# Performance work log

Measured on AMD Instinct MI355X. Metric: run time of the kernel, lower is better.

The kernel has to match this reference:

```python
import jax, jax.numpy as jnp
import numpy as np

B_, L_, H_, P_ = 8, 4096, 512, 256
DT_MIN, DT_MAX = 1e-3, 1e-1


def setup_inputs() -> dict:
    key = jax.random.key(0)
    ks = jax.random.split(key, 6)
    input_sequence = jax.random.normal(ks[0], (B_, L_, H_), jnp.float32)
    # Stable diagonal SSM eigenvalues (HiPPO-like): negative real, spread imaginary
    Lambda_re = -0.5 * jnp.ones((P_,), jnp.float32)
    Lambda_im = jnp.pi * jnp.arange(P_, dtype=jnp.float32)
    # B, C stored as real arrays with trailing real/imag channel, as in the module
    B = jax.random.normal(ks[1], (P_, H_, 2), jnp.float32) / np.sqrt(2.0 * H_)
    C = jax.random.normal(ks[2], (H_, P_, 2), jnp.float32) / np.sqrt(float(P_))
    D = jax.random.normal(ks[3], (H_,), jnp.float32)
    log_step = jax.random.uniform(ks[4], (P_,), jnp.float32,
                                  float(np.log(DT_MIN)), float(np.log(DT_MAX)))
    return dict(input_sequence=input_sequence, Lambda_re=Lambda_re,
                Lambda_im=Lambda_im, B=B, C=C, D=D, log_step=log_step)


def _scan_ssm(Lambda_bar, Bu):
    """Diagonal linear recurrence x_k = Lambda_bar * x_{k-1} + Bu_k via parallel scan.
    Lambda_bar: (P,) complex64; Bu: (L, P) complex64 -> xs: (L, P) complex64."""
    A = jnp.broadcast_to(Lambda_bar, Bu.shape)

    def binop(e_i, e_j):
        a_i, b_i = e_i
        a_j, b_j = e_j
        return a_j * a_i, a_j * b_i + b_j

    _, xs = jax.lax.associative_scan(binop, (A, Bu))
    return xs


def reference(input_sequence, Lambda_re, Lambda_im, B, C, D, log_step):
    # complex parameters (conj_sym=True, clip_eigs=False, zoh discretization)
    Lambda = (Lambda_re + 1j * Lambda_im).astype(jnp.complex64)        # (P,)
    B_tilde = (B[..., 0] + 1j * B[..., 1]).astype(jnp.complex64)       # (P, H)
    C_tilde = (C[..., 0] + 1j * C[..., 1]).astype(jnp.complex64)       # (H, P)
    step = jnp.exp(log_step)                                           # (P,)
    # ZOH: Lambda_bar = exp(Lambda*dt); B_bar = Lambda^{-1}(Lambda_bar - I) B
    Lambda_bar = jnp.exp(Lambda * step)                                # (P,)
    B_bar = ((1.0 / Lambda) * (Lambda_bar - 1.0))[:, None] * B_tilde   # (P, H)
    # project inputs into state space: (B, L, P)
    Bu = jnp.einsum('blh,ph->blp', input_sequence.astype(jnp.complex64), B_bar)
    xs = jax.vmap(lambda bu: _scan_ssm(Lambda_bar, bu))(Bu)            # (B, L, P)
    state = xs[:, -1, :]                                               # (B, P)
    # conj_sym=True -> output uses 2 * Re(C x)
    ys = 2.0 * jnp.einsum('blp,hp->blh', xs, C_tilde).real             # (B, L, H)
    out = ys + D * input_sequence                                      # D-skip
    return out, state
```

## Files before the change

### kernel.cpp

```cpp
#include <hip/hip_runtime.h>
#include <hip/hip_bf16.h>

#define Hh 512
#define Pp 256
#define Ll 4096
#define Bb 8
#define BL (Bb*Ll)
#define Sc 64
#define NC 64

typedef __attribute__((ext_vector_type(8))) __bf16 bf16x8;
typedef __attribute__((ext_vector_type(4))) float  floatx4;

#define LAM_OFF     0
#define LAMS64D_OFF 512
#define B1G_OFF     1024
#define B3G_OFF     (B1G_OFF + 65536)
#define UB16_OFF    (B3G_OFF + 65536)
#define BUB_OFF     (UB16_OFF + 4194304)
#define XSB_OFF     (BUB_OFF + 4194304)
#define AGG_OFF     (XSB_OFF + 4194304)

#define OUT_ELEMS 16777216

#define GLL16(g, l) __builtin_amdgcn_global_load_lds( \
    (const __attribute__((address_space(1))) void*)(g), \
    (__attribute__((address_space(3))) void*)(l), 16, 0, 0)

#define BAR_LGKM()  asm volatile("s_waitcnt lgkmcnt(0)\n\ts_barrier" ::: "memory")
#define BAR_VMN(n)  asm volatile("s_waitcnt vmcnt(" #n ")\n\ts_barrier" ::: "memory")

__device__ __forceinline__ float2 cmul(float2 a, float2 b) {
    return make_float2(a.x*b.x - a.y*b.y, a.x*b.y + a.y*b.x);
}
__device__ __forceinline__ void cfma(float2& acc, float2 a, float2 b) {
    acc.x = fmaf(a.x, b.x, acc.x); acc.x = fmaf(-a.y, b.y, acc.x);
    acc.y = fmaf(a.x, b.y, acc.y); acc.y = fmaf( a.y, b.x, acc.y);
}

__global__ void prep(const float* __restrict__ u,
                     const float* __restrict__ Bmat, const float* __restrict__ Cmat,
                     const float* __restrict__ Lre, const float* __restrict__ Lim,
                     const float* __restrict__ logstep, float2* __restrict__ ws) {
    int bid = blockIdx.x;
    if (bid < 8192) {
        long i = ((long)bid * 256 + threadIdx.x) * 8;
        float4 v0 = *(const float4*)(u + i);
        float4 v1 = *(const float4*)(u + i + 4);
        __align__(16) __hip_bfloat162 t[4];
        t[0] = __float22bfloat162_rn(make_float2(v0.x, v0.y));
        t[1] = __float22bfloat162_rn(make_float2(v0.z, v0.w));
        t[2] = __float22bfloat162_rn(make_float2(v1.x, v1.y));
        t[3] = __float22bfloat162_rn(make_float2(v1.z, v1.w));
        *(bf16x8*)((__hip_bfloat16*)(ws + UB16_OFF) + i) = *(const bf16x8*)t;
    } else if (bid < 8704) {
        int idx = (bid - 8192) * 256 + threadIdx.x;
        int p = idx >> 9, h = idx & 511;
        double lr = (double)Lre[p], li = (double)Lim[p];
        double st = exp((double)logstep[p]);
        double a  = lr * st, th = li * st;
        double er = exp(a);
        double lamr = er * cos(th), lami = er * sin(th);
        double nr = lamr - 1.0, ni = lami;
        double den = lr*lr + li*li;
        float gx = (float)((nr*lr + ni*li)/den), gy = (float)((ni*lr - nr*li)/den);
        float2 b = ((const float2*)Bmat)[idx];
        float re = gx*b.x - gy*b.y;
        float im = gx*b.y + gy*b.x;
        __hip_bfloat16* B1 = (__hip_bfloat16*)(ws + B1G_OFF);
        B1[(2*p)*512 + h]   = __float2bfloat16(re);
        B1[(2*p+1)*512 + h] = __float2bfloat16(im);
    } else if (bid < 9216) {
        int idx = (bid - 8704) * 256 + threadIdx.x;
        int h = idx >> 8, p = idx & 255;
        float2 c = ((const float2*)Cmat)[idx];
        __hip_bfloat162* B3 = (__hip_bfloat162*)(ws + B3G_OFF);
        B3[h*256 + p] = __float22bfloat162_rn(make_float2(2.f*c.x, -2.f*c.y));
    } else {
        int p = threadIdx.x;
        double lr = (double)Lre[p], li = (double)Lim[p];
        double st = exp((double)logstep[p]);
        double a  = lr * st, th = li * st;
        double er = exp(a);
        ws[LAM_OFF + p] = make_float2((float)(er*cos(th)), (float)(er*sin(th)));
        double er64 = exp(64.0 * a), th64 = 64.0 * th;
        ((double2*)(ws + LAMS64D_OFF))[p] = make_double2(er64*cos(th64), er64*sin(th64));
    }
}

#define STAGE(buf, kt) do { \
    _Pragma("unroll") \
    for (int h_ = 0; h_ < 2; ++h_) { \
        _Pragma("unroll") \
        for (int r_ = 0; r_ < 2; ++r_) { \
            GLL16(aSrc + (h_*128 + r_*64)*1024 + (kt)*128, \
                  ldsSt + (buf)*65536 + h_*16384 + r_*8192); \
            GLL16(bSrc + (h_*128 + r_*64)*1024 + (kt)*128, \
                  ldsSt + (buf)*65536 + 32768 + h_*16384 + r_*8192); \
        } \
    } \
} while (0)

template<int EPI>
__global__ __launch_bounds__(512, 2)
void gemm8(const __hip_bfloat16* __restrict__ A,
           const __hip_bfloat16* __restrict__ B,
           void* __restrict__ Cout,
           const __hip_bfloat16* __restrict__ ub,
           const float* __restrict__ Dv) {
    __shared__ __align__(16) char lds[131072];
    const int tid = threadIdx.x;
    const int w = tid >> 6, l = tid & 63;

    const int idx = blockIdx.x;
    const int swz = (idx & 7) * 32 + (idx >> 3);
    const int mt = swz >> 1, nt = swz & 1;
    const long M0 = (long)mt * 256;
    const int  N0 = nt * 256;

    const int rA  = l >> 3;
    const int csw = ((l & 7) ^ rA) * 16;
    const char* aSrc = (const char*)A + (M0 + w*8 + rA) * 1024 + csw;
    const char* bSrc = (const char*)B + (long)(N0 + w*8 + rA) * 1024 + csw;
    char* ldsSt = lds + w*1024 + l*16;

    const int quad = l >> 4, ml = l & 15, m7 = ml & 7;
    const int wm = w & 1, wn = w >> 1;
    const int o0 = ((quad    ) ^ m7) * 16;
    const int o1 = ((quad + 4) ^ m7) * 16;
    const char* aRd = lds + wm*16384 + ml*128;
    const char* bRd = lds + 32768 + (wn >> 1)*16384 + ((wn & 1)*64 + ml)*128;

    floatx4 acc[8][4];
    #pragma unroll
    for (int i = 0; i < 8; ++i)
        #pragma unroll
        for (int j = 0; j < 4; ++j) acc[i][j] = (floatx4)0.f;

    STAGE(0, 0);
    STAGE(1, 1);
    BAR_VMN(8);

    #pragma unroll
    for (int t = 0; t < 8; ++t) {
        const int tb = (t & 1) * 65536;

        {
            bf16x8 af[8], bfr[4];
            #pragma unroll
            for (int fm = 0; fm < 8; ++fm)
                af[fm] = *(const bf16x8*)(aRd + tb + fm*2048 + o0);
            #pragma unroll
            for (int fn = 0; fn < 4; ++fn)
                bfr[fn] = *(const bf16x8*)(bRd + tb + fn*2048 + o0);
            __builtin_amdgcn_s_setprio(1);
            #pragma unroll
            for (int fm = 0; fm < 8; ++fm)
                #pragma unroll
                for (int fn = 0; fn < 4; ++fn)
                    acc[fm][fn] = __builtin_amdgcn_mfma_f32_16x16x32_bf16(
                        af[fm], bfr[fn], acc[fm][fn], 0, 0, 0);
            __builtin_amdgcn_s_setprio(0);
        }

        {
            bf16x8 af[8], bfr[4];
            #pragma unroll
            for (int fm = 0; fm < 8; ++fm)
                af[fm] = *(const bf16x8*)(aRd + tb + fm*2048 + o1);
            #pragma unroll
            for (int fn = 0; fn < 4; ++fn)
                bfr[fn] = *(const bf16x8*)(bRd + tb + fn*2048 + o1);
            BAR_LGKM();
            if (t + 2 < 8) STAGE(t & 1, t + 2);
            __builtin_amdgcn_sched_barrier(0);
            __builtin_amdgcn_s_setprio(1);
            #pragma unroll
            for (int fm = 0; fm < 8; ++fm)
                #pragma unroll
                for (int fn = 0; fn < 4; ++fn)
                    acc[fm][fn] = __builtin_amdgcn_mfma_f32_16x16x32_bf16(
                        af[fm], bfr[fn], acc[fm][fn], 0, 0, 0);
            __builtin_amdgcn_s_setprio(0);
        }

        if (t < 6)       BAR_VMN(8);
        else if (t == 6) BAR_VMN(0);
    }

    #pragma unroll
    for (int fm = 0; fm < 8; ++fm)
        #pragma unroll
        for (int fn = 0; fn < 4; ++fn) {
            const int col = N0 + wn*64 + fn*16 + ml;
            const float d = (EPI == 1) ? Dv[col] : 0.f;
            #pragma unroll
            for (int reg = 0; reg < 4; ++reg) {
                const long row = M0 + wm*128 + fm*16 + quad*4 + reg;
                const long o = row * 512 + col;
                if (EPI == 0) {
                    ((__hip_bfloat16*)Cout)[o] = __float2bfloat16(acc[fm][fn][reg]);
                } else {
                    ((float*)Cout)[o] = acc[fm][fn][reg] + d * __bfloat162float(ub[o]);
                }
            }
        }
}

__global__ void k2a(float2* __restrict__ ws) {
    int p = threadIdx.x;
    int bc = blockIdx.x;
    int b = bc >> 6, c = bc & 63;
    float2 lam = ws[LAM_OFF + p];
    float2 lp[8];
    lp[0] = make_float2(1.f, 0.f);
    #pragma unroll
    for (int k = 1; k < 8; ++k) lp[k] = cmul(lp[k-1], lam);
    float2 lam8 = cmul(lp[7], lam);
    const __hip_bfloat162* __restrict__ bub = (const __hip_bfloat162*)(ws + BUB_OFF);
    long base = (long)(b*Ll + c*Sc) * Pp + p;
    float2 agg = make_float2(0.f, 0.f);
    for (int j0 = 0; j0 < Sc; j0 += 8) {
        float2 v[8];
        #pragma unroll
        for (int i = 0; i < 8; ++i)
            v[i] = __bfloat1622float2(bub[base + (long)(j0 + i) * Pp]);
        float2 s0 = make_float2(0.f, 0.f), s1 = make_float2(0.f, 0.f);
        #pragma unroll
        for (int i = 0; i < 8; i += 2) {
            cfma(s0, lp[7 - i], v[i]);
            cfma(s1, lp[6 - i], v[i + 1]);
        }
        float2 G = make_float2(s0.x + s1.x, s0.y + s1.y);
        float2 na = cmul(lam8, agg);
        agg = make_float2(na.x + G.x, na.y + G.y);
    }
    ws[AGG_OFF + bc * Pp + p] = agg;
}

__global__ void k2c(float2* __restrict__ ws, float* __restrict__ dout) {
    int p = threadIdx.x;
    int bc = blockIdx.x;
    int b = bc >> 6, c = bc & 63;
    float2 lam = ws[LAM_OFF + p];
    double2 l64 = ((const double2*)(ws + LAMS64D_OFF))[p];
    double cr = 0.0, ci = 0.0;
    for (int cp = 0; cp < c; ++cp) {
        float2 a = ws[AGG_OFF + (b*NC + cp) * Pp + p];
        double nr = fma(l64.x, cr, (double)a.x); nr = fma(-l64.y, ci, nr);
        double ni = fma(l64.x, ci, (double)a.y); ni = fma( l64.y, cr, ni);
        cr = nr; ci = ni;
    }
    float2 x = make_float2((float)cr, (float)ci);
    const __hip_bfloat162* __restrict__ bub = (const __hip_bfloat162*)(ws + BUB_OFF);
    __hip_bfloat162* __restrict__ xsb = (__hip_bfloat162*)(ws + XSB_OFF);
    long base = (long)(b*Ll + c*Sc) * Pp + p;
    for (int j0 = 0; j0 < Sc; j0 += 8) {
        float2 v[8];
        #pragma unroll
        for (int i = 0; i < 8; ++i)
            v[i] = __bfloat1622float2(bub[base + (long)(j0 + i) * Pp]);
        #pragma unroll
        for (int i = 0; i < 8; ++i) {
            float nr = fmaf(lam.x, x.x, v[i].x); nr = fmaf(-lam.y, x.y, nr);
            float ni = fmaf(lam.x, x.y, v[i].y); ni = fmaf( lam.y, x.x, ni);
            x.x = nr; x.y = ni;
            xsb[base + (long)(j0 + i) * Pp] = __float22bfloat162_rn(make_float2(x.x, x.y));
        }
    }
    if (c == NC - 1) {
        dout[OUT_ELEMS + b * Pp + p] = x.x;
        dout[OUT_ELEMS + Bb * Pp + b * Pp + p] = x.y;
    }
}

extern "C" void kernel_launch(void* const* d_in, const int* in_sizes, int n_in,
                              void* d_out, int out_size, void* d_ws, size_t ws_size,
                              hipStream_t stream) {
    const float* u       = (const float*)d_in[0];
    const float* Lre     = (const float*)d_in[1];
    const float* Lim     = (const float*)d_in[2];
    const float* Bmat    = (const float*)d_in[3];
    const float* Cmat    = (const float*)d_in[4];
    const float* Dv      = (const float*)d_in[5];
    const float* logstep = (const float*)d_in[6];
    float*  out = (float*)d_out;
    float2* ws  = (float2*)d_ws;

    prep<<<9217, 256, 0, stream>>>(u, Bmat, Cmat, Lre, Lim, logstep, ws);

    gemm8<0><<<256, 512, 0, stream>>>(
        (const __hip_bfloat16*)(ws + UB16_OFF),
        (const __hip_bfloat16*)(ws + B1G_OFF),
        (void*)(ws + BUB_OFF), nullptr, nullptr);

    k2a<<<Bb*NC, 256, 0, stream>>>(ws);
    k2c<<<Bb*NC, 256, 0, stream>>>(ws, out);

    gemm8<1><<<256, 512, 0, stream>>>(
        (const __hip_bfloat16*)(ws + XSB_OFF),
        (const __hip_bfloat16*)(ws + B3G_OFF),
        (void*)out,
        (const __hip_bfloat16*)(ws + UB16_OFF), Dv);
}
```

Measured before the change: 203.7 us.

## Fuse chunk-aggregate scan computation into first GEMM epilogue, drop k2a kernel

The per-chunk state aggregates are now computed inside the Bu GEMM epilogue, directly from the accumulator registers. Each lane weights its rows by powers of lambda and reduces across lanes with shuffles, then writes one aggregate per 64-step chunk. This removes the separate k2a launch and its re-read of the bf16 Bu buffer from global memory. In exchange the GEMM epilogue does more complex arithmetic and register work, which may lower occupancy or lengthen the tail. Summation order also changes, with lambda powers rebuilt from repeated multiplies.

```diff
diff --git a/kernel.cpp b/kernel.cpp
--- a/kernel.cpp
+++ b/kernel.cpp
@@ -107,7 +107,9 @@
            const __hip_bfloat16* __restrict__ B,
            void* __restrict__ Cout,
            const __hip_bfloat16* __restrict__ ub,
-           const float* __restrict__ Dv) {
+           const float* __restrict__ Dv,
+           const float2* __restrict__ lamTab,
+           float2* __restrict__ aggOut) {
     __shared__ __align__(16) char lds[131072];
     const int tid = threadIdx.x;
     const int w = tid >> 6, l = tid & 63;
@@ -188,54 +190,69 @@
         else if (t == 6) BAR_VMN(0);
     }
 
-    #pragma unroll
-    for (int fm = 0; fm < 8; ++fm)
+    if constexpr (EPI == 0) {
+        const int b   = (int)(M0 >> 12);
+        const int gc0 = (int)((M0 >> 6) & 63);
         #pragma unroll
         for (int fn = 0; fn < 4; ++fn) {
             const int col = N0 + wn*64 + fn*16 + ml;
-            const float d = (EPI == 1) ? Dv[col] : 0.f;
-            #pragma unroll
-            for (int reg = 0; reg < 4; ++reg) {
-                const long row = M0 + wm*128 + fm*16 + quad*4 + reg;
-                const long o = row * 512 + col;
-                if (EPI == 0) {
-                    ((__hip_bfloat16*)Cout)[o] = __float2bfloat16(acc[fm][fn][reg]);
-                } else {
+            const int p = col >> 1;
+            const float2 lam = lamTab[p];
+            const float2 one = make_float2(1.f, 0.f);
+            const float2 l2  = cmul(lam, lam);
+            const float2 l3  = cmul(l2, lam);
+            const float2 l4  = cmul(l2, l2);
+            const float2 l8  = cmul(l4, l4);
+            const float2 l12 = cmul(l8, l4);
+            const float2 l16 = cmul(l8, l8);
+            const float2 l32 = cmul(l16, l16);
+            const float2 l48 = cmul(l32, l16);
+            const float2 P4q = (quad==3) ? one : (quad==2) ? l4 : (quad==1) ? l8 : l12;
+            #pragma unroll
+            for (int c = 0; c < 2; ++c) {
+                float2 sc = make_float2(0.f, 0.f);
+                #pragma unroll
+                for (int a = 0; a < 4; ++a) {
+                    const int fm = c*4 + a;
+                    float vr[4];
+                    #pragma unroll
+                    for (int reg = 0; reg < 4; ++reg) {
+                        const long row = M0 + wm*128 + fm*16 + quad*4 + reg;
+                        __hip_bfloat16 hv = __float2bfloat16(acc[fm][fn][reg]);
+                        ((__hip_bfloat16*)Cout)[row * 512 + col] = hv;
+                        vr[reg] = __bfloat162float(hv);
+                    }
+                    float2 s;
+                    s.x = fmaf(l3.x, vr[0], fmaf(l2.x, vr[1], fmaf(lam.x, vr[2], vr[3])));
+                    s.y = fmaf(l3.y, vr[0], fmaf(l2.y, vr[1], lam.y * vr[2]));
+                    const float2 p16 = (a==3) ? one : (a==2) ? l16 : (a==1) ? l32 : l48;
+                    cfma(sc, cmul(p16, P4q), s);
+                }
+                sc.x += __shfl_xor(sc.x, 16); sc.y += __shfl_xor(sc.y, 16);
+                sc.x += __shfl_xor(sc.x, 32); sc.y += __shfl_xor(sc.y, 32);
+                const float ox = __shfl_xor(sc.x, 1);
+                const float oy = __shfl_xor(sc.y, 1);
+                if (quad == 0 && (ml & 1) == 0) {
+                    aggOut[(b*NC + gc0 + wm*2 + c) * Pp + p] =
+                        make_float2(sc.x - oy, sc.y + ox);
+                }
+            }
+        }
+    } else {
+        #pragma unroll
+        for (int fm = 0; fm < 8; ++fm)
+            #pragma unroll
+            for (int fn = 0; fn < 4; ++fn) {
+                const int col = N0 + wn*64 + fn*16 + ml;
+                const float d = Dv[col];
+                #pragma unroll
+                for (int reg = 0; reg < 4; ++reg) {
+                    const long row = M0 + wm*128 + fm*16 + quad*4 + reg;
+                    const long o = row * 512 + col;
                     ((float*)Cout)[o] = acc[fm][fn][reg] + d * __bfloat162float(ub[o]);
                 }
             }
-        }
-}
-
-__global__ void k2a(float2* __restrict__ ws) {
-    int p = threadIdx.x;
-    int bc = blockIdx.x;
-    int b = bc >> 6, c = bc & 63;
-    float2 lam = ws[LAM_OFF + p];
-    float2 lp[8];
-    lp[0] = make_float2(1.f, 0.f);
-    #pragma unroll
-    for (int k = 1; k < 8; ++k) lp[k] = cmul(lp[k-1], lam);
-    float2 lam8 = cmul(lp[7], lam);
-    const __hip_bfloat162* __restrict__ bub = (const __hip_bfloat162*)(ws + BUB_OFF);
-    long base = (long)(b*Ll + c*Sc) * Pp + p;
-    float2 agg = make_float2(0.f, 0.f);
-    for (int j0 = 0; j0 < Sc; j0 += 8) {
-        float2 v[8];
-        #pragma unroll
-        for (int i = 0; i < 8; ++i)
-            v[i] = __bfloat1622float2(bub[base + (long)(j0 + i) * Pp]);
-        float2 s0 = make_float2(0.f, 0.f), s1 = make_float2(0.f, 0.f);
-        #pragma unroll
-        for (int i = 0; i < 8; i += 2) {
-            cfma(s0, lp[7 - i], v[i]);
-            cfma(s1, lp[6 - i], v[i + 1]);
-        }
-        float2 G = make_float2(s0.x + s1.x, s0.y + s1.y);
-        float2 na = cmul(lam8, agg);
-        agg = make_float2(na.x + G.x, na.y + G.y);
-    }
-    ws[AGG_OFF + bc * Pp + p] = agg;
+    }
 }
 
 __global__ void k2c(float2* __restrict__ ws, float* __restrict__ dout) {
@@ -292,14 +309,15 @@
     gemm8<0><<<256, 512, 0, stream>>>(
         (const __hip_bfloat16*)(ws + UB16_OFF),
         (const __hip_bfloat16*)(ws + B1G_OFF),
-        (void*)(ws + BUB_OFF), nullptr, nullptr);
-
-    k2a<<<Bb*NC, 256, 0, stream>>>(ws);
+        (void*)(ws + BUB_OFF), nullptr, nullptr,
+        (const float2*)(ws + LAM_OFF), (float2*)(ws + AGG_OFF));
+
     k2c<<<Bb*NC, 256, 0, stream>>>(ws, out);
 
     gemm8<1><<<256, 512, 0, stream>>>(
         (const __hip_bfloat16*)(ws + XSB_OFF),
         (const __hip_bfloat16*)(ws + B3G_OFF),
         (void*)out,
-        (const __hip_bfloat16*)(ws + UB16_OFF), Dv);
-}
+        (const __hip_bfloat16*)(ws + UB16_OFF), Dv,
+        nullptr, nullptr);
+}
```

Measured after the change: 205.6 us. Within noise of the previous version (+0.9%).
